# Kernel optimization log

Hardware: AMD Instinct MI355X
Metric: run time of the kernel (lower is better)

## Reference

```python
import jax, jax.numpy as jnp
import numpy as np

NUM_G = 16
OFFSET = jnp.linspace(0.0, 8.0, NUM_G)
COEFF = -0.5 / (8.0 / (NUM_G - 1)) ** 2  # GaussianSmearing coeff
EPS = 1e-5

N_NODES, N_EDGES, F_IN, HID, N_CLS, N_LAYERS = 20000, 320000, 6, 128, 21, 4


def _layernorm(h, g, b):
    m = jnp.mean(h, axis=-1, keepdims=True)
    v = jnp.var(h, axis=-1, keepdims=True)
    return (h - m) * jax.lax.rsqrt(v + EPS) * g + b


def setup_inputs() -> dict:
    key = jax.random.key(0)
    ks = jax.random.split(key, 16)
    Z = 2 * HID + NUM_G  # CGConv concat dim = 272

    def lin_w(k, shape, fan_in):
        lim = 1.0 / np.sqrt(fan_in)
        return jax.random.uniform(k, shape, jnp.float32, -lim, lim)

    return {
        "x": jax.random.normal(ks[0], (N_NODES, F_IN), jnp.float32),
        "edge_index": jax.random.randint(ks[1], (2, N_EDGES), 0, N_NODES, jnp.int32),
        "edge_dist": jax.random.uniform(ks[2], (N_EDGES,), jnp.float32, 0.0, 8.0),
        "W_node": lin_w(ks[3], (F_IN, HID), F_IN),
        "b_node": jnp.zeros((HID,), jnp.float32),
        "Wf": lin_w(ks[4], (N_LAYERS, Z, HID), Z),
        "bf": jnp.zeros((N_LAYERS, HID), jnp.float32),
        "Ws": lin_w(ks[5], (N_LAYERS, Z, HID), Z),
        "bs": jnp.zeros((N_LAYERS, HID), jnp.float32),
        "bn_g": jnp.ones((N_LAYERS, HID), jnp.float32),
        "bn_b": jnp.zeros((N_LAYERS, HID), jnp.float32),
        "ln_g": jnp.ones((N_LAYERS, HID), jnp.float32),
        "ln_b": jnp.zeros((N_LAYERS, HID), jnp.float32),
        "lnout_g": jnp.ones((HID,), jnp.float32),
        "lnout_b": jnp.zeros((HID,), jnp.float32),
        "W_fc": lin_w(ks[6], (HID, N_CLS), HID),
        "b_fc": jnp.zeros((N_CLS,), jnp.float32),
    }


def reference(x, edge_index, edge_dist, W_node, b_node, Wf, bf, Ws, bs,
              bn_g, bn_b, ln_g, ln_b, lnout_g, lnout_b, W_fc, b_fc):
    # edge RBF expansion: [E, 16]
    e = jnp.exp(COEFF * (edge_dist[:, None] - OFFSET[None, :]) ** 2)
    # node embedding: [N, H]
    h = x @ W_node + b_node
    src, dst = edge_index[0], edge_index[1]  # PyG: messages flow src (x_j) -> dst (x_i)
    n = h.shape[0]
    for l in range(Wf.shape[0]):
        # CGConv message: z = [x_i, x_j, e]; m = sigmoid(lin_f(z)) * softplus(lin_s(z))
        z = jnp.concatenate([h[dst], h[src], e], axis=-1)            # [E, 2H+16]
        msg = jax.nn.sigmoid(z @ Wf[l] + bf[l]) * jax.nn.softplus(z @ Ws[l] + bs[l])
        agg = jax.ops.segment_sum(msg, dst, num_segments=n)          # [N, H]
        # BatchNorm1d (training-mode batch stats) on aggregated messages
        mu = jnp.mean(agg, axis=0)
        var = jnp.var(agg, axis=0)
        agg = (agg - mu) * jax.lax.rsqrt(var + EPS) * bn_g[l] + bn_b[l]
        conv_out = agg + h                                           # CGConv residual
        # block: LayerNorm -> ReLU -> (dropout=identity in eval) -> + identity
        h = jax.nn.relu(_layernorm(conv_out, ln_g[l], ln_b[l])) + h
    h = _layernorm(h, lnout_g, lnout_b)
    return h @ W_fc + b_fc
```

## Files before the change

### kernel.cpp

```cpp
#include <hip/hip_runtime.h>
#include <hip/hip_fp16.h>
#include <math.h>

#define HID 128
#define NUMG 16
#define ZDIM 272
#define NCLS 21
#define LN_EPS 1e-5f
#define DELTA (8.0f/15.0f)
#define RBFC  (-1.7578125f)
#define NBINS 4096
#define LOG2E 1.44269504f
#define LN2F  0.69314718f

typedef _Float16 half8  __attribute__((ext_vector_type(8)));
typedef _Float16 half4t __attribute__((ext_vector_type(4)));
typedef float    floatx4 __attribute__((ext_vector_type(4)));

#if __has_builtin(__builtin_amdgcn_exp2f)
#define EXP2(x) __builtin_amdgcn_exp2f(x)
#else
#define EXP2(x) __expf(LN2F*(x))
#endif
#if __has_builtin(__builtin_amdgcn_logf)
#define LOG2(x) __builtin_amdgcn_logf(x)
#else
#define LOG2(x) (LOG2E*__logf(x))
#endif

__device__ __forceinline__ float frcp(float x){ return __builtin_amdgcn_rcpf(x); }

__launch_bounds__(256)
__global__ void preproc_kernel(const float* __restrict__ Wf, const float* __restrict__ Ws,
                               const float* __restrict__ bf, const float* __restrict__ bs,
                               _Float16* __restrict__ Wm16, float* __restrict__ Bias2,
                               _Float16* __restrict__ T,
                               const float* __restrict__ x, const float* __restrict__ Wn,
                               const float* __restrict__ bn, float* __restrict__ h, int N){
  __shared__ float sW[16][256];
  __shared__ float sR[16][16];
  int b = blockIdx.x;
  int t = threadIdx.x;
  if (b < 1024){
    int idx = b*256 + t;
    {
      int l    = idx >> 16;
      int lane = (idx >> 3) & 63;
      int j    = idx & 7;
      int kb   = (idx >> 14) & 3;
      int tt   = (idx >> 9) & 31;
      int k    = kb*32 + ((lane >> 4) << 3) + j;
      int c    = tt*16 + (lane & 15);
      int row  = (c < 256) ? k : 128 + k;
      int cc   = (c < 256) ? c : c - 256;
      int f    = cc >> 1;
      const float* Wsel = ((c & 1) ? Ws : Wf) + l*ZDIM*HID;
      Wm16[idx] = (_Float16)Wsel[row*HID + f];
    }
    if (idx < 4*256){
      int l = idx >> 8; int c = idx & 255;
      Bias2[idx] = ((c & 1) ? bs : bf)[l*HID + (c >> 1)];
    }
  } else if (b < 2048){
    int bb   = b - 1024;
    int l    = bb >> 8;
    int bin0 = (bb & 255) * 16;
    for (int i = t; i < 16*256; i += 256){
      int k = i >> 8; int p = i & 255;
      int s = p & 1; int feat = (p >> 2) + ((p & 2) ? 64 : 0);
      const float* W = (s ? Ws : Wf) + l*ZDIM*HID;
      sW[k][p] = W[(256+k)*HID + feat];
    }
    {
      int bi = t >> 4; int k = t & 15;
      float d = 8.0f * (float)(bin0 + bi) / (float)(NBINS-1);
      float xx = d - (float)k * DELTA;
      sR[bi][k] = __expf(RBFC*xx*xx);
    }
    __syncthreads();
    for (int i = t; i < 16*256; i += 256){
      int bi = i >> 8; int p = i & 255;
      float acc = 0.f;
      #pragma unroll
      for (int k=0;k<16;k++) acc += sR[bi][k]*sW[k][p];
      T[((size_t)l*NBINS + bin0 + bi)*256 + p] = (_Float16)(acc*LOG2E);
    }
  } else {
    int idx = (b - 2048)*256 + t;
    if (idx < N*HID){
      int n = idx >> 7; int f = idx & 127;
      float acc = bn[f];
      const float* xr = x + n*6;
      #pragma unroll
      for (int k=0;k<6;k++) acc += xr[k]*Wn[k*HID+f];
      h[idx] = acc;
    }
  }
}


__global__ void hist_kernel(const int* __restrict__ ei, int* __restrict__ deg, int E){
  int e = blockIdx.x*256 + threadIdx.x;
  if (e >= E) return;
  atomicAdd(&deg[ei[E + e]], 1);
}

__global__ void scan_partial(const int* __restrict__ deg, int* __restrict__ bsum, int N){
  int t = threadIdx.x;
  int i = blockIdx.x*256 + t;
  int v = (i < N) ? deg[i] : 0;
  #pragma unroll
  for (int m=32;m;m>>=1) v += __shfl_xor(v, m, 64);
  __shared__ int ws[4];
  if ((t & 63) == 0) ws[t>>6] = v;
  __syncthreads();
  if (t == 0) bsum[blockIdx.x] = ws[0]+ws[1]+ws[2]+ws[3];
}

__global__ void scan_bsum(int* __restrict__ bsum, int nb){
  __shared__ int sm[256];
  int t = threadIdx.x;
  int v = (t < nb) ? bsum[t] : 0;
  sm[t] = v; __syncthreads();
  #pragma unroll
  for (int off=1; off<256; off<<=1){
    int add = (t >= off) ? sm[t-off] : 0;
    __syncthreads();
    sm[t] += add;
    __syncthreads();
  }
  if (t < nb) bsum[t] = sm[t] - v;
}

__global__ void scan_write(const int* __restrict__ deg, const int* __restrict__ bsum,
                           int* __restrict__ rowptr, int* __restrict__ cursor, int N, int E){
  __shared__ int sm[256];
  int t = threadIdx.x;
  int i = blockIdx.x*256 + t;
  int v = (i < N) ? deg[i] : 0;
  sm[t] = v; __syncthreads();
  #pragma unroll
  for (int off=1; off<256; off<<=1){
    int add = (t >= off) ? sm[t-off] : 0;
    __syncthreads();
    sm[t] += add;
    __syncthreads();
  }
  if (i < N){
    int ex = bsum[blockIdx.x] + sm[t] - v;
    rowptr[i] = ex; cursor[i] = ex;
  }
  if (i == 0) rowptr[N] = E;
}

__global__ void scatter_kernel(const int* __restrict__ ei, const float* __restrict__ dist,
                               int* __restrict__ cursor, int2* __restrict__ edata, int E){
  int e = blockIdx.x*256 + threadIdx.x;
  if (e >= E) return;
  int dst = ei[E + e];
  int pos = atomicAdd(&cursor[dst], 1);
  float d = dist[e];
  int b = (int)(d * ((float)(NBINS-1) / 8.0f) + 0.5f);
  if (b > NBINS-1) b = NBINS-1;
  if (b < 0) b = 0;
  edata[pos] = make_int2(ei[e]*256, b*256);
}


__launch_bounds__(256)
__global__ void node_gemm0_kernel(const float* __restrict__ h, const _Float16* __restrict__ Wm,
                                  const float* __restrict__ Bias2, _Float16* __restrict__ Pdst,
                                  _Float16* __restrict__ Psrc, float* __restrict__ bn_zero, int N){
  if (blockIdx.x == 0){ for (int i=threadIdx.x;i<1024;i+=256) bn_zero[i]=0.f; }
  int lane = threadIdx.x & 63;
  int w    = threadIdx.x >> 6;
  int m0   = blockIdx.x * 16;
  int arow = m0 + (lane & 15);
  int kbase= (lane >> 4) * 8;
  floatx4 acc[8];
  #pragma unroll
  for (int t=0;t<8;t++) acc[t] = (floatx4){0.f,0.f,0.f,0.f};
  #pragma unroll
  for (int kb=0; kb<4; kb++){
    const float* ap = h + arow*HID + kb*32 + kbase;
    float4 a0 = *(const float4*)ap;
    float4 a1 = *(const float4*)(ap+4);
    half8 af;
    af[0]=(_Float16)a0.x; af[1]=(_Float16)a0.y; af[2]=(_Float16)a0.z; af[3]=(_Float16)a0.w;
    af[4]=(_Float16)a1.x; af[5]=(_Float16)a1.y; af[6]=(_Float16)a1.z; af[7]=(_Float16)a1.w;
    const _Float16* bp = Wm + ((kb*32 + w*8)*64 + lane)*8;
    #pragma unroll
    for (int t=0;t<8;t++){
      half8 b8 = *(const half8*)(bp + t*512);
      acc[t] = __builtin_amdgcn_mfma_f32_16x16x32_f16(af, b8, acc[t], 0,0,0);
    }
  }
  int quad = lane >> 4;
  int cl   = lane & 15;
  int hi2  = (w & 1) ? 2 : 0;
  if (w < 2){
    #pragma unroll
    for (int t=0;t<8;t++){
      int cp = t*16 + cl;
      int c  = (w&1)*128 + cp;
      int p  = ((cp >> 1) << 2) + hi2 + (cp & 1);
      float b2 = Bias2[c];
      #pragma unroll
      for (int r=0;r<4;r++)
        Pdst[(m0 + quad*4 + r)*256 + p] = (_Float16)((acc[t][r] + b2)*LOG2E);
    }
  } else {
    #pragma unroll
    for (int t=0;t<8;t++){
      int cp = t*16 + cl;
      int p  = ((cp >> 1) << 2) + hi2 + (cp & 1);
      #pragma unroll
      for (int r=0;r<4;r++)
        Psrc[(m0 + quad*4 + r)*256 + p] = (_Float16)(acc[t][r]*LOG2E);
    }
  }
}

__launch_bounds__(256)
__global__ void fused_apply_gemm(const float2* __restrict__ agg2, float* __restrict__ h,
                                 const float* __restrict__ bn_in, float* __restrict__ bn_zero,
                                 const float* __restrict__ bng, const float* __restrict__ bnb,
                                 const float* __restrict__ lng, const float* __restrict__ lnb,
                                 float invN,
                                 const _Float16* __restrict__ Wm, const float* __restrict__ Bias2,
                                 _Float16* __restrict__ Pdst, _Float16* __restrict__ Psrc, int N){
  __shared__ float sh[16][132];
  int t = threadIdx.x;
  if (blockIdx.x == 0){ for (int i=t;i<1024;i+=256) bn_zero[i]=0.f; }
  int lane = t & 63, w = t >> 6;
  int f0 = lane, f1 = lane + 64;
  float sm0=0.f,sq0=0.f,sm1=0.f,sq1=0.f;
  #pragma unroll
  for (int s=0;s<4;s++){
    sm0 += bn_in[s*256 + 2*lane];
    sm1 += bn_in[s*256 + 2*lane + 1];
    sq0 += bn_in[s*256 + 128 + 2*lane];
    sq1 += bn_in[s*256 + 129 + 2*lane];
  }
  float mu0 = sm0*invN, mu1 = sm1*invN;
  float rv0 = rsqrtf(sq0*invN - mu0*mu0 + LN_EPS);
  float rv1 = rsqrtf(sq1*invN - mu1*mu1 + LN_EPS);
  float G0 = bng[f0], B0 = bnb[f0], G1 = bng[f1], B1 = bnb[f1];
  float Lg0 = lng[f0], Lb0 = lnb[f0], Lg1 = lng[f1], Lb1 = lnb[f1];
  int row0 = blockIdx.x*16;
  #pragma unroll
  for (int i=0;i<4;i++){
    int rr = w*4 + i; int row = row0 + rr;
    float2 a = agg2[row*64 + lane];
    float h0 = h[row*HID + f0], h1 = h[row*HID + f1];
    float c0 = (a.x - mu0)*rv0*G0 + B0 + h0;
    float c1 = (a.y - mu1)*rv1*G1 + B1 + h1;
    float s = c0 + c1, q = c0*c0 + c1*c1;
    #pragma unroll
    for (int m=32;m;m>>=1){ s += __shfl_xor(s,m,64); q += __shfl_xor(q,m,64); }
    float mean = s*(1.0f/128.0f);
    float var  = q*(1.0f/128.0f) - mean*mean;
    float r = rsqrtf(var + LN_EPS);
    float n0 = fmaxf((c0-mean)*r*Lg0 + Lb0, 0.f) + h0;
    float n1 = fmaxf((c1-mean)*r*Lg1 + Lb1, 0.f) + h1;
    h[row*HID + f0] = n0; h[row*HID + f1] = n1;
    sh[rr][f0] = n0; sh[rr][f1] = n1;
  }
  __syncthreads();
  int arl  = lane & 15;
  int kbase= (lane >> 4) * 8;
  floatx4 acc[8];
  #pragma unroll
  for (int k=0;k<8;k++) acc[k] = (floatx4){0.f,0.f,0.f,0.f};
  #pragma unroll
  for (int kb=0; kb<4; kb++){
    const float* ap = &sh[arl][kb*32 + kbase];
    float4 a0 = *(const float4*)ap;
    float4 a1 = *(const float4*)(ap+4);
    half8 af;
    af[0]=(_Float16)a0.x; af[1]=(_Float16)a0.y; af[2]=(_Float16)a0.z; af[3]=(_Float16)a0.w;
    af[4]=(_Float16)a1.x; af[5]=(_Float16)a1.y; af[6]=(_Float16)a1.z; af[7]=(_Float16)a1.w;
    const _Float16* bp = Wm + ((kb*32 + w*8)*64 + lane)*8;
    #pragma unroll
    for (int k=0;k<8;k++){
      half8 b8 = *(const half8*)(bp + k*512);
      acc[k] = __builtin_amdgcn_mfma_f32_16x16x32_f16(af, b8, acc[k], 0,0,0);
    }
  }
  int quad = lane >> 4;
  int cl   = lane & 15;
  int hi2  = (w & 1) ? 2 : 0;
  int m0   = row0;
  if (w < 2){
    #pragma unroll
    for (int k=0;k<8;k++){
      int cp = k*16 + cl;
      int c  = (w&1)*128 + cp;
      int p  = ((cp >> 1) << 2) + hi2 + (cp & 1);
      float b2 = Bias2[c];
      #pragma unroll
      for (int r=0;r<4;r++)
        Pdst[(m0 + quad*4 + r)*256 + p] = (_Float16)((acc[k][r] + b2)*LOG2E);
    }
  } else {
    #pragma unroll
    for (int k=0;k<8;k++){
      int cp = k*16 + cl;
      int p  = ((cp >> 1) << 2) + hi2 + (cp & 1);
      #pragma unroll
      for (int r=0;r<4;r++)
        Psrc[(m0 + quad*4 + r)*256 + p] = (_Float16)(acc[k][r]*LOG2E);
    }
  }
}

__launch_bounds__(256)
__global__ void agg_kernel(const _Float16* __restrict__ Pdst, const _Float16* __restrict__ Psrc,
                           const int2* __restrict__ edata, const int* __restrict__ rowptr,
                           const _Float16* __restrict__ T,
                           float2* __restrict__ agg2){
  int lane = threadIdx.x & 63;
  int w    = threadIdx.x >> 6;
  int half = lane >> 5;
  int hl   = lane & 31;
  int l8   = hl * 8;
  int node = blockIdx.x*4 + w;
  half8 ad8 = *(const half8*)(Pdst + node*256 + l8);
  floatx4 acc = (floatx4){0.f,0.f,0.f,0.f};
  int beg = rowptr[node], end = rowptr[node+1];
  #pragma unroll 2
  for (int j = beg + half; j < end; j += 2){
    int2 ed = edata[j];
    half8 p8 = *(const half8*)(Psrc + ed.x + l8);
    half8 t8 = *(const half8*)(T + ed.y + l8);
    half8 z = p8 + ad8 + t8;
    float xf0=(float)z[0], xs0=(float)z[1], xf1=(float)z[2], xs1=(float)z[3];
    float xf2=(float)z[4], xs2=(float)z[5], xf3=(float)z[6], xs3=(float)z[7];
    float g0  = frcp(1.f + EXP2(-xf0));
    float sp0 = fmaxf(xs0, 0.f) + LOG2(1.f + EXP2(-fabsf(xs0)));
    float g1  = frcp(1.f + EXP2(-xf1));
    float sp1 = fmaxf(xs1, 0.f) + LOG2(1.f + EXP2(-fabsf(xs1)));
    float g2  = frcp(1.f + EXP2(-xf2));
    float sp2 = fmaxf(xs2, 0.f) + LOG2(1.f + EXP2(-fabsf(xs2)));
    float g3  = frcp(1.f + EXP2(-xf3));
    float sp3 = fmaxf(xs3, 0.f) + LOG2(1.f + EXP2(-fabsf(xs3)));
    acc[0] = fmaf(g0, sp0, acc[0]);
    acc[1] = fmaf(g1, sp1, acc[1]);
    acc[2] = fmaf(g2, sp2, acc[2]);
    acc[3] = fmaf(g3, sp3, acc[3]);
  }
  #pragma unroll
  for (int c=0;c<4;c++) acc[c] += __shfl_xor(acc[c], 32, 64);
  int col = (hl << 1) | half;
  float2 outv = half ? make_float2(acc[2]*LN2F, acc[3]*LN2F)
                     : make_float2(acc[0]*LN2F, acc[1]*LN2F);
  agg2[node*64 + col] = outv;
}

__global__ void bnstats_kernel(const float* __restrict__ agg, float* __restrict__ bnstat, int N){
  int f = threadIdx.x;
  float s = 0.f, q = 0.f;
  for (int r = blockIdx.x; r < N; r += gridDim.x){
    float v = agg[r*HID + f];
    s += v; q += v*v;
  }
  float* sb = bnstat + ((blockIdx.x & 3) << 8);
  atomicAdd(sb + f,       s);
  atomicAdd(sb + 128 + f, q);
}

__launch_bounds__(256)
__global__ void lnfc_kernel(const float2* __restrict__ agg2, const float* __restrict__ h,
                            const float* __restrict__ bn_in,
                            const float* __restrict__ bng, const float* __restrict__ bnb,
                            const float* __restrict__ lng, const float* __restrict__ lnb,
                            float invN,
                            const float* __restrict__ g, const float* __restrict__ b,
                            const float* __restrict__ Wfc, const float* __restrict__ bfc,
                            float* __restrict__ out, int N){
  __shared__ float sh[16][132];
  __shared__ float wl[HID*NCLS];
  __shared__ float bl[NCLS];
  int t = threadIdx.x;
  for (int i = t; i < HID*NCLS; i += 256) wl[i] = Wfc[i];
  if (t < NCLS) bl[t] = bfc[t];
  int lane = t & 63, w = t >> 6;
  int f0 = lane, f1 = lane + 64;
  float sm0=0.f,sq0=0.f,sm1=0.f,sq1=0.f;
  #pragma unroll
  for (int s=0;s<4;s++){
    sm0 += bn_in[s*256 + 2*lane];
    sm1 += bn_in[s*256 + 2*lane + 1];
    sq0 += bn_in[s*256 + 128 + 2*lane];
    sq1 += bn_in[s*256 + 129 + 2*lane];
  }
  float mu0 = sm0*invN, mu1 = sm1*invN;
  float rv0 = rsqrtf(sq0*invN - mu0*mu0 + LN_EPS);
  float rv1 = rsqrtf(sq1*invN - mu1*mu1 + LN_EPS);
  float G0 = bng[f0], B0 = bnb[f0], G1 = bng[f1], B1 = bnb[f1];
  float Lg0 = lng[f0], Lb0 = lnb[f0], Lg1 = lng[f1], Lb1 = lnb[f1];
  float Fg0 = g[f0], Fb0 = b[f0], Fg1 = g[f1], Fb1 = b[f1];
  int row0 = blockIdx.x*16;
  #pragma unroll
  for (int i=0;i<4;i++){
    int rr = w*4 + i; int row = row0 + rr;
    float2 a = agg2[row*64 + lane];
    float h0 = h[row*HID + f0], h1 = h[row*HID + f1];
    float c0 = (a.x - mu0)*rv0*G0 + B0 + h0;
    float c1 = (a.y - mu1)*rv1*G1 + B1 + h1;
    float s = c0 + c1, q = c0*c0 + c1*c1;
    #pragma unroll
    for (int m=32;m;m>>=1){ s += __shfl_xor(s,m,64); q += __shfl_xor(q,m,64); }
    float mean = s*(1.0f/128.0f);
    float var  = q*(1.0f/128.0f) - mean*mean;
    float r = rsqrtf(var + LN_EPS);
    float n0 = fmaxf((c0-mean)*r*Lg0 + Lb0, 0.f) + h0;
    float n1 = fmaxf((c1-mean)*r*Lg1 + Lb1, 0.f) + h1;
    float s2 = n0 + n1, q2 = n0*n0 + n1*n1;
    #pragma unroll
    for (int m=32;m;m>>=1){ s2 += __shfl_xor(s2,m,64); q2 += __shfl_xor(q2,m,64); }
    float mean2 = s2*(1.0f/128.0f);
    float var2  = q2*(1.0f/128.0f) - mean2*mean2;
    float r2 = rsqrtf(var2 + LN_EPS);
    sh[rr][f0] = (n0-mean2)*r2*Fg0 + Fb0;
    sh[rr][f1] = (n1-mean2)*r2*Fg1 + Fb1;
  }
  __syncthreads();
  for (int idx = t; idx < 16*NCLS; idx += 256){
    int r = idx / NCLS, c = idx - r*NCLS;
    int orow = row0 + r;
    if (orow < N){
      float acc = bl[c];
      #pragma unroll 4
      for (int k=0;k<HID;k++) acc += sh[r][k]*wl[k*NCLS + c];
      out[orow*NCLS + c] = acc;
    }
  }
}


extern "C" void kernel_launch(void* const* d_in, const int* in_sizes, int n_in,
                              void* d_out, int out_size, void* d_ws, size_t ws_size,
                              hipStream_t stream){
  const float* x    = (const float*)d_in[0];
  const int*   ei   = (const int*)  d_in[1];
  const float* dist = (const float*)d_in[2];
  const float* Wn   = (const float*)d_in[3];
  const float* bn   = (const float*)d_in[4];
  const float* Wf   = (const float*)d_in[5];
  const float* bf   = (const float*)d_in[6];
  const float* Ws   = (const float*)d_in[7];
  const float* bs   = (const float*)d_in[8];
  const float* bng  = (const float*)d_in[9];
  const float* bnb  = (const float*)d_in[10];
  const float* lng  = (const float*)d_in[11];
  const float* lnb  = (const float*)d_in[12];
  const float* lnog = (const float*)d_in[13];
  const float* lnob = (const float*)d_in[14];
  const float* Wfc  = (const float*)d_in[15];
  const float* bfc  = (const float*)d_in[16];
  float* out = (float*)d_out;

  const int N = in_sizes[0] / 6;
  const int E = in_sizes[2];
  const int NB = (N + 255)/256;

  char* p = (char*)d_ws;
  auto alloc = [&](size_t bytes)->void*{
    void* r = (void*)p;
    p += (bytes + 255) & ~(size_t)255;
    return r;
  };
  float*     h      = (float*)    alloc((size_t)N*HID*4);
  _Float16*  Pdst   = (_Float16*) alloc((size_t)N*256*2);
  _Float16*  Psrc   = (_Float16*) alloc((size_t)N*256*2);
  float2*    agg2   = (float2*)   alloc((size_t)N*64*8);
  _Float16*  Wm16   = (_Float16*) alloc((size_t)4*65536*2);
  float*     Bias2  = (float*)    alloc((size_t)4*256*4);
  _Float16*  T      = (_Float16*) alloc((size_t)4*NBINS*256*2);
  float*     bnstat = (float*)    alloc((size_t)2*1024*4);
  int*       deg    = (int*)      alloc((size_t)N*4);
  int*       rowptr = (int*)      alloc((size_t)(N+1)*4);
  int*       cursor = (int*)      alloc((size_t)N*4);
  int*       bsum   = (int*)      alloc((size_t)NB*4);
  int2*      edata  = (int2*)     alloc((size_t)E*8);

  hipMemsetAsync(deg, 0, (size_t)N*4, stream);
  preproc_kernel<<<2048 + (N*HID + 255)/256, 256, 0, stream>>>(
      Wf, Ws, bf, bs, Wm16, Bias2, T, x, Wn, bn, h, N);
  hist_kernel<<<(E + 255)/256, 256, 0, stream>>>(ei, deg, E);
  scan_partial<<<NB, 256, 0, stream>>>(deg, bsum, N);
  scan_bsum<<<1, 256, 0, stream>>>(bsum, NB);
  scan_write<<<NB, 256, 0, stream>>>(deg, bsum, rowptr, cursor, N, E);
  scatter_kernel<<<(E + 255)/256, 256, 0, stream>>>(ei, dist, cursor, edata, E);

  float invN = 1.0f / (float)N;

  node_gemm0_kernel<<<N/16, 256, 0, stream>>>(
      h, Wm16, Bias2, Pdst, Psrc, bnstat, N);
  agg_kernel<<<N/4, 256, 0, stream>>>(
      Pdst, Psrc, edata, rowptr, T, agg2);
  bnstats_kernel<<<1024, 128, 0, stream>>>((const float*)agg2, bnstat, N);

  for (int l = 1; l < 4; l++){
    float* bn_in   = bnstat + ((l-1)&1)*1024;
    float* bn_next = bnstat + (l&1)*1024;
    fused_apply_gemm<<<N/16, 256, 0, stream>>>(
        agg2, h, bn_in, bn_next,
        bng + (l-1)*HID, bnb + (l-1)*HID, lng + (l-1)*HID, lnb + (l-1)*HID, invN,
        Wm16 + (size_t)l*65536, Bias2 + (size_t)l*256, Pdst, Psrc, N);
    agg_kernel<<<N/4, 256, 0, stream>>>(
        Pdst, Psrc, edata, rowptr, T + (size_t)l*NBINS*256, agg2);
    bnstats_kernel<<<1024, 128, 0, stream>>>((const float*)agg2, bn_next, N);
  }

  lnfc_kernel<<<N/16, 256, 0, stream>>>(
      agg2, h, bnstat + 1024,
      bng + 3*HID, bnb + 3*HID, lng + 3*HID, lnb + 3*HID, invN,
      lnog, lnob, Wfc, bfc, out, N);
}
```

Baseline: 416.2 us.

## Fuse degree histogram into preproc and unroll agg gather with contiguous halves

```diff
diff --git a/kernel.cpp b/kernel.cpp
--- a/kernel.cpp
+++ b/kernel.cpp
@@ -36,7 +36,9 @@
                                _Float16* __restrict__ Wm16, float* __restrict__ Bias2,
                                _Float16* __restrict__ T,
                                const float* __restrict__ x, const float* __restrict__ Wn,
-                               const float* __restrict__ bn, float* __restrict__ h, int N){
+                               const float* __restrict__ bn, float* __restrict__ h,
+                               const int* __restrict__ ei, int* __restrict__ deg,
+                               int N, int E, int nhb){
   __shared__ float sW[16][256];
   __shared__ float sR[16][16];
   int b = blockIdx.x;
@@ -85,7 +87,7 @@
       for (int k=0;k<16;k++) acc += sR[bi][k]*sW[k][p];
       T[((size_t)l*NBINS + bin0 + bi)*256 + p] = (_Float16)(acc*LOG2E);
     }
-  } else {
+  } else if (b < 2048 + nhb){
     int idx = (b - 2048)*256 + t;
     if (idx < N*HID){
       int n = idx >> 7; int f = idx & 127;
@@ -95,15 +97,12 @@
       for (int k=0;k<6;k++) acc += xr[k]*Wn[k*HID+f];
       h[idx] = acc;
     }
-  }
-}
-
-
-__global__ void hist_kernel(const int* __restrict__ ei, int* __restrict__ deg, int E){
-  int e = blockIdx.x*256 + threadIdx.x;
-  if (e >= E) return;
-  atomicAdd(&deg[ei[E + e]], 1);
-}
+  } else {
+    int e = (b - 2048 - nhb)*256 + t;
+    if (e < E) atomicAdd(&deg[ei[E + e]], 1);
+  }
+}
+
 
 __global__ void scan_partial(const int* __restrict__ deg, int* __restrict__ bsum, int N){
   int t = threadIdx.x;
@@ -328,26 +327,46 @@
   half8 ad8 = *(const half8*)(Pdst + node*256 + l8);
   floatx4 acc = (floatx4){0.f,0.f,0.f,0.f};
   int beg = rowptr[node], end = rowptr[node+1];
-  #pragma unroll 2
-  for (int j = beg + half; j < end; j += 2){
-    int2 ed = edata[j];
-    half8 p8 = *(const half8*)(Psrc + ed.x + l8);
-    half8 t8 = *(const half8*)(T + ed.y + l8);
+  int len  = end - beg;
+  int len0 = (len + 1) >> 1;
+  int s = beg + half*len0;
+  int e = half ? end : (beg + len0);
+
+  auto body = [&](half8 p8, half8 t8, float vm){
     half8 z = p8 + ad8 + t8;
     float xf0=(float)z[0], xs0=(float)z[1], xf1=(float)z[2], xs1=(float)z[3];
     float xf2=(float)z[4], xs2=(float)z[5], xf3=(float)z[6], xs3=(float)z[7];
-    float g0  = frcp(1.f + EXP2(-xf0));
+    float g0  = vm*frcp(1.f + EXP2(-xf0));
     float sp0 = fmaxf(xs0, 0.f) + LOG2(1.f + EXP2(-fabsf(xs0)));
-    float g1  = frcp(1.f + EXP2(-xf1));
+    float g1  = vm*frcp(1.f + EXP2(-xf1));
     float sp1 = fmaxf(xs1, 0.f) + LOG2(1.f + EXP2(-fabsf(xs1)));
-    float g2  = frcp(1.f + EXP2(-xf2));
+    float g2  = vm*frcp(1.f + EXP2(-xf2));
     float sp2 = fmaxf(xs2, 0.f) + LOG2(1.f + EXP2(-fabsf(xs2)));
-    float g3  = frcp(1.f + EXP2(-xf3));
+    float g3  = vm*frcp(1.f + EXP2(-xf3));
     float sp3 = fmaxf(xs3, 0.f) + LOG2(1.f + EXP2(-fabsf(xs3)));
     acc[0] = fmaf(g0, sp0, acc[0]);
     acc[1] = fmaf(g1, sp1, acc[1]);
     acc[2] = fmaf(g2, sp2, acc[2]);
     acc[3] = fmaf(g3, sp3, acc[3]);
+  };
+
+  for (int j0 = s; j0 < e; j0 += 4){
+    int j1 = j0+1 < e ? j0+1 : e-1;
+    int j2 = j0+2 < e ? j0+2 : e-1;
+    int j3 = j0+3 < e ? j0+3 : e-1;
+    int2 ed0 = edata[j0], ed1 = edata[j1], ed2 = edata[j2], ed3 = edata[j3];
+    half8 p0 = *(const half8*)(Psrc + ed0.x + l8);
+    half8 t0 = *(const half8*)(T    + ed0.y + l8);
+    half8 p1 = *(const half8*)(Psrc + ed1.x + l8);
+    half8 t1 = *(const half8*)(T    + ed1.y + l8);
+    half8 p2 = *(const half8*)(Psrc + ed2.x + l8);
+    half8 t2 = *(const half8*)(T    + ed2.y + l8);
+    half8 p3 = *(const half8*)(Psrc + ed3.x + l8);
+    half8 t3 = *(const half8*)(T    + ed3.y + l8);
+    body(p0, t0, 1.f);
+    body(p1, t1, (j0+1 < e) ? 1.f : 0.f);
+    body(p2, t2, (j0+2 < e) ? 1.f : 0.f);
+    body(p3, t3, (j0+3 < e) ? 1.f : 0.f);
   }
   #pragma unroll
   for (int c=0;c<4;c++) acc[c] += __shfl_xor(acc[c], 32, 64);
@@ -464,6 +483,8 @@
   const int N = in_sizes[0] / 6;
   const int E = in_sizes[2];
   const int NB = (N + 255)/256;
+  const int nhb = (N*HID + 255)/256;
+  const int neb = (E + 255)/256;
 
   char* p = (char*)d_ws;
   auto alloc = [&](size_t bytes)->void*{
@@ -486,13 +507,12 @@
   int2*      edata  = (int2*)     alloc((size_t)E*8);
 
   hipMemsetAsync(deg, 0, (size_t)N*4, stream);
-  preproc_kernel<<<2048 + (N*HID + 255)/256, 256, 0, stream>>>(
-      Wf, Ws, bf, bs, Wm16, Bias2, T, x, Wn, bn, h, N);
-  hist_kernel<<<(E + 255)/256, 256, 0, stream>>>(ei, deg, E);
+  preproc_kernel<<<2048 + nhb + neb, 256, 0, stream>>>(
+      Wf, Ws, bf, bs, Wm16, Bias2, T, x, Wn, bn, h, ei, deg, N, E, nhb);
   scan_partial<<<NB, 256, 0, stream>>>(deg, bsum, N);
   scan_bsum<<<1, 256, 0, stream>>>(bsum, NB);
   scan_write<<<NB, 256, 0, stream>>>(deg, bsum, rowptr, cursor, N, E);
-  scatter_kernel<<<(E + 255)/256, 256, 0, stream>>>(ei, dist, cursor, edata, E);
+  scatter_kernel<<<neb, 256, 0, stream>>>(ei, dist, cursor, edata, E);
 
   float invN = 1.0f / (float)N;
 
```

Measured after the change: 416.1 us. About the same (-0.0%).
